# Kernel optimization log

Hardware: AMD Instinct MI355X
Metric: run time of the kernel (lower is better)

## Reference

```python
import jax, jax.numpy as jnp
import numpy as np

N_NODES = 100000


def gcn_conv(x, W, b, src, dst, num_nodes):
    """PyG GCNConv: out = D^{-1/2} (A + I) D^{-1/2} (x W) + b, messages src->dst."""
    h = x @ W  # [N, out]
    # degree with self-loops (edge weight 1)
    deg = jax.ops.segment_sum(jnp.ones(src.shape[0], dtype=x.dtype), dst,
                              num_segments=num_nodes) + 1.0
    dinv = jax.lax.rsqrt(deg)  # [N]
    norm = dinv[src] * dinv[dst]  # [E]
    msg = h[src] * norm[:, None]  # gather + scale, [E, out]
    agg = jax.ops.segment_sum(msg, dst, num_segments=num_nodes)
    # self-loop term: norm_ii = dinv[i]^2
    agg = agg + h * (dinv * dinv)[:, None]
    return agg + b


def setup_inputs() -> dict:
    key = jax.random.key(0)
    ks = jax.random.split(key, 9)
    N, F_in, H1, H2, C = N_NODES, 128, 64, 32, 10
    E = 3200000
    feature = jax.random.normal(ks[0], (N, F_in), dtype=jnp.float32)
    edge_index = jax.random.randint(ks[1], (2, E), 0, N, dtype=jnp.int64)
    def glorot(k, shape):
        lim = np.sqrt(6.0 / (shape[0] + shape[1]))
        return jax.random.uniform(k, shape, jnp.float32, -lim, lim)
    return {
        "feature": feature,
        "edge_index": edge_index,
        "W1": glorot(ks[2], (F_in, H1)),
        "b1": jnp.zeros((H1,), jnp.float32),
        "W2": glorot(ks[3], (H1, H2)),
        "b2": jnp.zeros((H2,), jnp.float32),
        "Wc": glorot(ks[4], (H2, C)),
        "bc": jnp.zeros((C,), jnp.float32),
    }


def reference(feature, edge_index, W1, b1, W2, b2, Wc, bc):
    src, dst = edge_index[0], edge_index[1]
    x = gcn_conv(feature, W1, b1, src, dst, N_NODES)
    x = jax.nn.relu(x)
    # dropout is identity in eval mode
    x = gcn_conv(x, W2, b2, src, dst, N_NODES)
    x = jax.nn.relu(x)
    logits = x @ Wc + bc
    return jax.nn.log_softmax(logits, axis=1)
```

## Files before the change

### kernel.cpp

```cpp
#include <hip/hip_runtime.h>

#define N_NODES 100000
#define F_IN 128
#define H1 64
#define H2 32
#define NCLS 10

#define BS_N 256
#define NBUCK ((N_NODES + BS_N - 1) / BS_N)
#define LCAP 32
#define MCAP 9216
#define OVCAP 6144
#define STCAP 9216
#define BIN_WG 256

__device__ __forceinline__ unsigned short f2bf(float f) {
    unsigned int u = __float_as_uint(f);
    return (unsigned short)((u + 0x7fffu + ((u >> 16) & 1u)) >> 16);
}
__device__ __forceinline__ float bf2f(unsigned short u) {
    return __uint_as_float((unsigned int)u << 16);
}
__device__ __forceinline__ void accp(float* a, unsigned int u) {
    a[0] += __uint_as_float(u << 16);
    a[1] += __uint_as_float(u & 0xffff0000u);
}
__device__ __forceinline__ void accp4(float* a, uint4 v) {
    accp(a + 0, v.x); accp(a + 2, v.y); accp(a + 4, v.z); accp(a + 6, v.w);
}

__global__ __launch_bounds__(512) void bin_kernel(const int* __restrict__ src,
                                                  const int* __restrict__ dst, int E,
                                                  unsigned int* __restrict__ gcur,
                                                  unsigned int* __restrict__ mainr,
                                                  unsigned int* __restrict__ ovcnt,
                                                  unsigned int* __restrict__ ovbuf) {
    __shared__ unsigned int buf[NBUCK][LCAP];
    __shared__ int cnt[NBUCK];
    int tid = threadIdx.x;
    for (int b = tid; b < NBUCK; b += 512) cnt[b] = 0;

    int chunk = (E + gridDim.x - 1) / gridDim.x;
    int e_lo = blockIdx.x * chunk;
    int e_hi = min(e_lo + chunk, E);

    int d0 = 0, s0 = 0, d1 = 0, s1 = 0;
    {
        int ea = e_lo + tid, eb = e_lo + 512 + tid;
        if (ea < e_hi) { d0 = dst[ea]; s0 = src[ea]; }
        if (eb < e_hi) { d1 = dst[eb]; s1 = src[eb]; }
    }
    __syncthreads();

    for (int base = e_lo; base < e_hi; base += 1024) {
        if (base + tid < e_hi) {
            int b = d0 >> 8;
            unsigned int en = ((unsigned int)s0 << 8) | (unsigned int)(d0 & 255);
            int p = atomicAdd(&cnt[b], 1);
            if (p < LCAP) buf[b][p] = en;
            else {
                unsigned int op = atomicAdd(&ovcnt[b * 16], 1u);
                if (op < OVCAP) ovbuf[(size_t)b * OVCAP + op] = en;
            }
        }
        if (base + 512 + tid < e_hi) {
            int b = d1 >> 8;
            unsigned int en = ((unsigned int)s1 << 8) | (unsigned int)(d1 & 255);
            int p = atomicAdd(&cnt[b], 1);
            if (p < LCAP) buf[b][p] = en;
            else {
                unsigned int op = atomicAdd(&ovcnt[b * 16], 1u);
                if (op < OVCAP) ovbuf[(size_t)b * OVCAP + op] = en;
            }
        }
        __syncthreads();
        {
            int nb = base + 1024;
            int ea = nb + tid, eb = nb + 512 + tid;
            if (ea < e_hi) { d0 = dst[ea]; s0 = src[ea]; }
            if (eb < e_hi) { d1 = dst[eb]; s1 = src[eb]; }
        }
        for (int b = tid; b < NBUCK; b += 512) {
            int c = cnt[b]; if (c > LCAP) c = LCAP;
            int nf = c & ~15;
            if (nf) {
                unsigned int gb = atomicAdd(&gcur[b * 16], (unsigned int)nf);
                if (gb + (unsigned)nf <= MCAP) {
                    for (int k = 0; k < nf; k += 4) {
                        uint4 v = make_uint4(buf[b][k], buf[b][k + 1],
                                             buf[b][k + 2], buf[b][k + 3]);
                        *(uint4*)&mainr[(size_t)b * MCAP + gb + k] = v;
                    }
                } else {
                    unsigned int op = atomicAdd(&ovcnt[b * 16], (unsigned int)nf);
                    for (int k = 0; k < nf; ++k)
                        if (op + k < OVCAP) ovbuf[(size_t)b * OVCAP + op + k] = buf[b][k];
                }
                int rem = c - nf;
                for (int k = 0; k < rem; ++k) buf[b][k] = buf[b][nf + k];
                cnt[b] = rem;
            } else {
                cnt[b] = c;
            }
        }
        __syncthreads();
    }
    for (int b = tid; b < NBUCK; b += 512) {
        int c = cnt[b]; if (c > LCAP) c = LCAP;
        if (c) {
            unsigned int ob = atomicAdd(&ovcnt[b * 16], (unsigned int)c);
            for (int k = 0; k < c; ++k)
                if (ob + k < OVCAP) ovbuf[(size_t)b * OVCAP + ob + k] = buf[b][k];
        }
    }
}

__global__ __launch_bounds__(256) void build_kernel(const unsigned int* __restrict__ gcur,
                                                    unsigned int* __restrict__ mainr,
                                                    const unsigned int* __restrict__ ovcnt,
                                                    const unsigned int* __restrict__ ovbuf,
                                                    float* __restrict__ dinv,
                                                    int* __restrict__ row_start,
                                                    int* __restrict__ row_end) {
    __shared__ unsigned int stage[STCAP];
    __shared__ int degl[BS_N];
    __shared__ int rs_l[BS_N];
    __shared__ int curl[BS_N];
    __shared__ int wtot[4];
    int b = blockIdx.x;
    int tid = threadIdx.x;

    int cm = (int)gcur[b * 16]; if (cm > MCAP) cm = MCAP;
    for (int i = tid; i < cm; i += 256) stage[i] = mainr[(size_t)b * MCAP + i];
    int co = (int)ovcnt[b * 16]; if (co > OVCAP) co = OVCAP;
    for (int i = tid; i < co; i += 256) {
        int p = cm + i;
        if (p < STCAP) stage[p] = ovbuf[(size_t)b * OVCAP + i];
    }
    int c = cm + co; if (c > STCAP) c = STCAP;
    degl[tid] = 0;
    __syncthreads();

    for (int i = tid; i < c; i += 256) atomicAdd(&degl[stage[i] & 255], 1);
    __syncthreads();

    int lane = tid & 63, w = tid >> 6;
    int d = degl[tid];
    int x = d;
    #pragma unroll
    for (int off = 1; off < 64; off <<= 1) {
        int y = __shfl_up(x, off);
        if (lane >= off) x += y;
    }
    if (lane == 63) wtot[w] = x;
    __syncthreads();
    int pbase = 0;
    #pragma unroll
    for (int k = 0; k < 4; ++k) if (k < w) pbase += wtot[k];
    rs_l[tid] = pbase + x - d;
    curl[tid] = 0;
    __syncthreads();

    size_t gbase = (size_t)b * MCAP;
    for (int i = tid; i < c; i += 256) {
        unsigned int en = stage[i];
        int dl = en & 255;
        int p = atomicAdd(&curl[dl], 1);
        mainr[gbase + rs_l[dl] + p] = en >> 8;
    }
    int node = b * BS_N + tid;
    if (node < N_NODES) {
        int deg = degl[tid];
        dinv[node] = rsqrtf((float)deg + 1.0f);
        row_start[node] = (int)gbase + rs_l[tid];
        row_end[node] = (int)gbase + rs_l[tid] + deg;
    }
}

__global__ __launch_bounds__(256) void gemm1_kernel(const float* __restrict__ X,
                                                    const float* __restrict__ W,
                                                    const float* __restrict__ dinv,
                                                    unsigned short* __restrict__ H) {
    __shared__ float Xs[64][68];
    __shared__ float Ws[F_IN * H1];
    int r0 = blockIdx.x * 64;
    const float4* W4 = (const float4*)W;
    float4* Ws4 = (float4*)Ws;
    for (int i = threadIdx.x; i < F_IN * H1 / 4; i += 256) Ws4[i] = W4[i];

    int tx = threadIdx.x & 15;
    int ty = threadIdx.x >> 4;
    float acc[4][4] = {};

    for (int kh = 0; kh < 2; ++kh) {
        __syncthreads();
        for (int it = 0; it < 4; ++it) {
            int idx = threadIdx.x + it * 256;
            int r = idx >> 4, k4 = idx & 15;
            int row = r0 + r;
            float4 v = (row < N_NODES)
                ? ((const float4*)X)[(size_t)row * 32 + kh * 16 + k4]
                : make_float4(0.f, 0.f, 0.f, 0.f);
            *(float4*)&Xs[r][k4 * 4] = v;
        }
        __syncthreads();
        #pragma unroll 8
        for (int k = 0; k < 64; ++k) {
            float4 wb = *(const float4*)&Ws[(kh * 64 + k) * H1 + tx * 4];
            float xa0 = Xs[ty * 4 + 0][k];
            float xa1 = Xs[ty * 4 + 1][k];
            float xa2 = Xs[ty * 4 + 2][k];
            float xa3 = Xs[ty * 4 + 3][k];
            acc[0][0] += xa0 * wb.x; acc[0][1] += xa0 * wb.y; acc[0][2] += xa0 * wb.z; acc[0][3] += xa0 * wb.w;
            acc[1][0] += xa1 * wb.x; acc[1][1] += xa1 * wb.y; acc[1][2] += xa1 * wb.z; acc[1][3] += xa1 * wb.w;
            acc[2][0] += xa2 * wb.x; acc[2][1] += xa2 * wb.y; acc[2][2] += xa2 * wb.z; acc[2][3] += xa2 * wb.w;
            acc[3][0] += xa3 * wb.x; acc[3][1] += xa3 * wb.y; acc[3][2] += xa3 * wb.z; acc[3][3] += xa3 * wb.w;
        }
    }
    #pragma unroll
    for (int i = 0; i < 4; ++i) {
        int row = r0 + ty * 4 + i;
        if (row < N_NODES) {
            float dv = dinv[row];
            unsigned int lo = (unsigned int)f2bf(acc[i][0] * dv) |
                              ((unsigned int)f2bf(acc[i][1] * dv) << 16);
            unsigned int hi = (unsigned int)f2bf(acc[i][2] * dv) |
                              ((unsigned int)f2bf(acc[i][3] * dv) << 16);
            *(uint2*)&H[(size_t)row * H1 + tx * 4] = make_uint2(lo, hi);
        }
    }
}

__global__ __launch_bounds__(256) void gemm2_kernel(const float* __restrict__ X,
                                                    const float* __restrict__ W,
                                                    const float* __restrict__ dinv,
                                                    unsigned short* __restrict__ H) {
    __shared__ float Xs[64][68];
    __shared__ float Ws[H1 * H2];
    int r0 = blockIdx.x * 64;
    const float4* W4 = (const float4*)W;
    float4* Ws4 = (float4*)Ws;
    for (int i = threadIdx.x; i < H1 * H2 / 4; i += 256) Ws4[i] = W4[i];
    for (int it = 0; it < 4; ++it) {
        int idx = threadIdx.x + it * 256;
        int r = idx >> 4, k4 = idx & 15;
        int row = r0 + r;
        float4 v = (row < N_NODES)
            ? ((const float4*)X)[(size_t)row * 16 + k4]
            : make_float4(0.f, 0.f, 0.f, 0.f);
        *(float4*)&Xs[r][k4 * 4] = v;
    }
    __syncthreads();
    int tx = threadIdx.x & 15;
    int ty = threadIdx.x >> 4;
    float acc[4][2] = {};
    #pragma unroll 8
    for (int k = 0; k < 64; ++k) {
        float2 wb = *(const float2*)&Ws[k * H2 + tx * 2];
        float xa0 = Xs[ty * 4 + 0][k];
        float xa1 = Xs[ty * 4 + 1][k];
        float xa2 = Xs[ty * 4 + 2][k];
        float xa3 = Xs[ty * 4 + 3][k];
        acc[0][0] += xa0 * wb.x; acc[0][1] += xa0 * wb.y;
        acc[1][0] += xa1 * wb.x; acc[1][1] += xa1 * wb.y;
        acc[2][0] += xa2 * wb.x; acc[2][1] += xa2 * wb.y;
        acc[3][0] += xa3 * wb.x; acc[3][1] += xa3 * wb.y;
    }
    #pragma unroll
    for (int i = 0; i < 4; ++i) {
        int row = r0 + ty * 4 + i;
        if (row < N_NODES) {
            float dv = dinv[row];
            unsigned int v = (unsigned int)f2bf(acc[i][0] * dv) |
                             ((unsigned int)f2bf(acc[i][1] * dv) << 16);
            *(unsigned int*)&H[(size_t)row * H2 + tx * 2] = v;
        }
    }
}

__global__ __launch_bounds__(256) void pull1_kernel(const unsigned short* __restrict__ h,
                                                    const unsigned int* __restrict__ csr,
                                                    const int* __restrict__ row_start,
                                                    const int* __restrict__ row_end,
                                                    const float* __restrict__ dinv,
                                                    const float* __restrict__ b,
                                                    float* __restrict__ xout) {
    int wave = (blockIdx.x * 256 + threadIdx.x) >> 6;
    int lane = threadIdx.x & 63;
    int g = lane >> 3;
    int sub = lane & 7;
    int i = wave;
    int e0 = row_start[i], e1 = row_end[i];
    float acc[8] = {};
    int e = e0;
    for (; e + 16 <= e1; e += 16) {
        int s0 = csr[e + g];
        int s1 = csr[e + 8 + g];
        uint4 v0 = *(const uint4*)&h[(size_t)s0 * H1 + sub * 8];
        uint4 v1 = *(const uint4*)&h[(size_t)s1 * H1 + sub * 8];
        accp4(acc, v0);
        accp4(acc, v1);
    }
    if (e + 8 <= e1) {
        int s = csr[e + g];
        uint4 v = *(const uint4*)&h[(size_t)s * H1 + sub * 8];
        accp4(acc, v);
        e += 8;
    }
    if (e < e1) {
        int idx = e + g;
        if (idx < e1) {
            int s = csr[idx];
            uint4 v = *(const uint4*)&h[(size_t)s * H1 + sub * 8];
            accp4(acc, v);
        }
    }
    #pragma unroll
    for (int m = 8; m < 64; m <<= 1) {
        #pragma unroll
        for (int j = 0; j < 8; ++j) acc[j] += __shfl_xor(acc[j], m);
    }
    if (g == 0) {
        float di = dinv[i];
        uint4 sv = *(const uint4*)&h[(size_t)i * H1 + sub * 8];
        accp4(acc, sv);
        float4 o0, o1;
        o0.x = fmaxf(di * acc[0] + b[sub * 8 + 0], 0.0f);
        o0.y = fmaxf(di * acc[1] + b[sub * 8 + 1], 0.0f);
        o0.z = fmaxf(di * acc[2] + b[sub * 8 + 2], 0.0f);
        o0.w = fmaxf(di * acc[3] + b[sub * 8 + 3], 0.0f);
        o1.x = fmaxf(di * acc[4] + b[sub * 8 + 4], 0.0f);
        o1.y = fmaxf(di * acc[5] + b[sub * 8 + 5], 0.0f);
        o1.z = fmaxf(di * acc[6] + b[sub * 8 + 6], 0.0f);
        o1.w = fmaxf(di * acc[7] + b[sub * 8 + 7], 0.0f);
        *(float4*)&xout[(size_t)i * H1 + sub * 8] = o0;
        *(float4*)&xout[(size_t)i * H1 + sub * 8 + 4] = o1;
    }
}

__global__ __launch_bounds__(256) void pull2_kernel(const unsigned short* __restrict__ h,
                                                    const unsigned int* __restrict__ csr,
                                                    const int* __restrict__ row_start,
                                                    const int* __restrict__ row_end,
                                                    const float* __restrict__ dinv,
                                                    const float* __restrict__ b,
                                                    float* __restrict__ xout) {
    int wave = (blockIdx.x * 256 + threadIdx.x) >> 6;
    int lane = threadIdx.x & 63;
    int g = lane >> 2;
    int sub = lane & 3;
    int i = wave;
    int e0 = row_start[i], e1 = row_end[i];
    float acc[8] = {};
    int e = e0;
    for (; e + 32 <= e1; e += 32) {
        int s0 = csr[e + g];
        int s1 = csr[e + 16 + g];
        uint4 v0 = *(const uint4*)&h[(size_t)s0 * H2 + sub * 8];
        uint4 v1 = *(const uint4*)&h[(size_t)s1 * H2 + sub * 8];
        accp4(acc, v0);
        accp4(acc, v1);
    }
    if (e + 16 <= e1) {
        int s = csr[e + g];
        uint4 v = *(const uint4*)&h[(size_t)s * H2 + sub * 8];
        accp4(acc, v);
        e += 16;
    }
    if (e < e1) {
        int idx = e + g;
        if (idx < e1) {
            int s = csr[idx];
            uint4 v = *(const uint4*)&h[(size_t)s * H2 + sub * 8];
            accp4(acc, v);
        }
    }
    #pragma unroll
    for (int m = 4; m < 64; m <<= 1) {
        #pragma unroll
        for (int j = 0; j < 8; ++j) acc[j] += __shfl_xor(acc[j], m);
    }
    if (g == 0) {
        float di = dinv[i];
        uint4 sv = *(const uint4*)&h[(size_t)i * H2 + sub * 8];
        accp4(acc, sv);
        float4 o0, o1;
        o0.x = fmaxf(di * acc[0] + b[sub * 8 + 0], 0.0f);
        o0.y = fmaxf(di * acc[1] + b[sub * 8 + 1], 0.0f);
        o0.z = fmaxf(di * acc[2] + b[sub * 8 + 2], 0.0f);
        o0.w = fmaxf(di * acc[3] + b[sub * 8 + 3], 0.0f);
        o1.x = fmaxf(di * acc[4] + b[sub * 8 + 4], 0.0f);
        o1.y = fmaxf(di * acc[5] + b[sub * 8 + 5], 0.0f);
        o1.z = fmaxf(di * acc[6] + b[sub * 8 + 6], 0.0f);
        o1.w = fmaxf(di * acc[7] + b[sub * 8 + 7], 0.0f);
        *(float4*)&xout[(size_t)i * H2 + sub * 8] = o0;
        *(float4*)&xout[(size_t)i * H2 + sub * 8 + 4] = o1;
    }
}

__global__ __launch_bounds__(256) void final_kernel(const float* __restrict__ X2,
                                                    const float* __restrict__ Wc,
                                                    const float* __restrict__ bc,
                                                    float* __restrict__ out) {
    __shared__ float Ws[H2 * NCLS];
    __shared__ float bs[NCLS];
    for (int idx = threadIdx.x; idx < H2 * NCLS; idx += 256) Ws[idx] = Wc[idx];
    if (threadIdx.x < NCLS) bs[threadIdx.x] = bc[threadIdx.x];
    __syncthreads();
    int i = blockIdx.x * blockDim.x + threadIdx.x;
    if (i >= N_NODES) return;
    float x[H2];
    #pragma unroll
    for (int k = 0; k < H2; ++k) x[k] = X2[(size_t)i * H2 + k];
    float lg[NCLS];
    #pragma unroll
    for (int c = 0; c < NCLS; ++c) {
        float acc = bs[c];
        #pragma unroll
        for (int k = 0; k < H2; ++k) acc += x[k] * Ws[k * NCLS + c];
        lg[c] = acc;
    }
    float m = lg[0];
    #pragma unroll
    for (int c = 1; c < NCLS; ++c) m = fmaxf(m, lg[c]);
    float s = 0.0f;
    #pragma unroll
    for (int c = 0; c < NCLS; ++c) s += expf(lg[c] - m);
    float lse = m + logf(s);
    #pragma unroll
    for (int c = 0; c < NCLS; ++c) out[(size_t)i * NCLS + c] = lg[c] - lse;
}

extern "C" void kernel_launch(void* const* d_in, const int* in_sizes, int n_in,
                              void* d_out, int out_size, void* d_ws, size_t ws_size,
                              hipStream_t stream) {
    const float* feature = (const float*)d_in[0];
    const int*   eidx    = (const int*)d_in[1];
    const float* W1      = (const float*)d_in[2];
    const float* b1      = (const float*)d_in[3];
    const float* W2      = (const float*)d_in[4];
    const float* b2      = (const float*)d_in[5];
    const float* Wc      = (const float*)d_in[6];
    const float* bc      = (const float*)d_in[7];
    float* out = (float*)d_out;

    const int E = in_sizes[1] / 2;
    const int* src = eidx;
    const int* dst = eidx + E;

    float*          ws        = (float*)d_ws;
    float*          dinv      = ws;
    int*            row_start = (int*)(dinv + N_NODES);
    int*            row_end   = row_start + N_NODES;
    unsigned int*   gcur      = (unsigned int*)(row_end + N_NODES);
    unsigned int*   ovcnt     = gcur + (size_t)NBUCK * 16;
    unsigned int*   ovbuf     = ovcnt + (size_t)NBUCK * 16;
    unsigned int*   mainr     = ovbuf + (size_t)NBUCK * OVCAP;
    unsigned short* h1b       = (unsigned short*)(mainr + (size_t)NBUCK * MCAP);
    float*          x1        = (float*)(h1b + (size_t)N_NODES * H1);
    unsigned short* h2b       = h1b;
    float*          x2        = x1;

    hipMemsetAsync(gcur, 0, (size_t)NBUCK * 32 * sizeof(unsigned int), stream);
    bin_kernel<<<BIN_WG, 512, 0, stream>>>(src, dst, E, gcur, mainr, ovcnt, ovbuf);
    build_kernel<<<NBUCK, 256, 0, stream>>>(gcur, mainr, ovcnt, ovbuf,
                                            dinv, row_start, row_end);

    gemm1_kernel<<<(N_NODES + 63) / 64, 256, 0, stream>>>(feature, W1, dinv, h1b);
    {
        unsigned int grid = (unsigned int)(((size_t)N_NODES * 64 + 255) / 256);
        pull1_kernel<<<grid, 256, 0, stream>>>(h1b, mainr, row_start, row_end, dinv, b1, x1);
    }

    gemm2_kernel<<<(N_NODES + 63) / 64, 256, 0, stream>>>(x1, W2, dinv, h2b);
    {
        unsigned int grid = (unsigned int)(((size_t)N_NODES * 64 + 255) / 256);
        pull2_kernel<<<grid, 256, 0, stream>>>(h2b, mainr, row_start, row_end, dinv, b2, x2);
    }

    final_kernel<<<(N_NODES + 255) / 256, 256, 0, stream>>>(x2, Wc, bc, out);
}
```

Before: 311.4 us.

## Fuse classifier and log-softmax into second aggregation; flush bin leftovers to main region

```diff
diff --git a/kernel.cpp b/kernel.cpp
--- a/kernel.cpp
+++ b/kernel.cpp
@@ -9,17 +9,15 @@
 #define BS_N 256
 #define NBUCK ((N_NODES + BS_N - 1) / BS_N)
 #define LCAP 32
-#define MCAP 9216
-#define OVCAP 6144
-#define STCAP 9216
+#define MCAP 12288
+#define OVCAP 2048
+#define STCAP 12288
 #define BIN_WG 256
+#define SENT 0xFFFFFFFFu
 
 __device__ __forceinline__ unsigned short f2bf(float f) {
     unsigned int u = __float_as_uint(f);
     return (unsigned short)((u + 0x7fffu + ((u >> 16) & 1u)) >> 16);
-}
-__device__ __forceinline__ float bf2f(unsigned short u) {
-    return __uint_as_float((unsigned int)u << 16);
 }
 __device__ __forceinline__ void accp(float* a, unsigned int u) {
     a[0] += __uint_as_float(u << 16);
@@ -108,9 +106,20 @@
     for (int b = tid; b < NBUCK; b += 512) {
         int c = cnt[b]; if (c > LCAP) c = LCAP;
         if (c) {
-            unsigned int ob = atomicAdd(&ovcnt[b * 16], (unsigned int)c);
-            for (int k = 0; k < c; ++k)
-                if (ob + k < OVCAP) ovbuf[(size_t)b * OVCAP + ob + k] = buf[b][k];
+            int cp = (c + 15) & ~15;
+            for (int k = c; k < cp; ++k) buf[b][k] = SENT;
+            unsigned int gb = atomicAdd(&gcur[b * 16], (unsigned int)cp);
+            if (gb + (unsigned)cp <= MCAP) {
+                for (int k = 0; k < cp; k += 4) {
+                    uint4 v = make_uint4(buf[b][k], buf[b][k + 1],
+                                         buf[b][k + 2], buf[b][k + 3]);
+                    *(uint4*)&mainr[(size_t)b * MCAP + gb + k] = v;
+                }
+            } else {
+                unsigned int op = atomicAdd(&ovcnt[b * 16], (unsigned int)c);
+                for (int k = 0; k < c; ++k)
+                    if (op + k < OVCAP) ovbuf[(size_t)b * OVCAP + op + k] = buf[b][k];
+            }
         }
     }
 }
@@ -141,7 +150,10 @@
     degl[tid] = 0;
     __syncthreads();
 
-    for (int i = tid; i < c; i += 256) atomicAdd(&degl[stage[i] & 255], 1);
+    for (int i = tid; i < c; i += 256) {
+        unsigned int en = stage[i];
+        if (en != SENT) atomicAdd(&degl[en & 255], 1);
+    }
     __syncthreads();
 
     int lane = tid & 63, w = tid >> 6;
@@ -164,9 +176,11 @@
     size_t gbase = (size_t)b * MCAP;
     for (int i = tid; i < c; i += 256) {
         unsigned int en = stage[i];
-        int dl = en & 255;
-        int p = atomicAdd(&curl[dl], 1);
-        mainr[gbase + rs_l[dl] + p] = en >> 8;
+        if (en != SENT) {
+            int dl = en & 255;
+            int p = atomicAdd(&curl[dl], 1);
+            mainr[gbase + rs_l[dl] + p] = en >> 8;
+        }
     }
     int node = b * BS_N + tid;
     if (node < N_NODES) {
@@ -343,8 +357,22 @@
                                                     const int* __restrict__ row_start,
                                                     const int* __restrict__ row_end,
                                                     const float* __restrict__ dinv,
-                                                    const float* __restrict__ b,
-                                                    float* __restrict__ xout) {
+                                                    const float* __restrict__ b2,
+                                                    const float* __restrict__ Wc,
+                                                    const float* __restrict__ bc,
+                                                    float* __restrict__ out) {
+    __shared__ float Wcs[336];
+    __shared__ float b2s[32];
+    __shared__ float bcs[16];
+    for (int t = threadIdx.x; t < 336; t += 256)
+        Wcs[t] = (t < H2 * NCLS) ? Wc[t] : 0.0f;
+    {
+        int t = threadIdx.x;
+        if (t < 32) b2s[t] = b2[t];
+        if (t < 16) bcs[t] = (t < NCLS) ? bc[t] : 0.0f;
+    }
+    __syncthreads();
+
     int wave = (blockIdx.x * 256 + threadIdx.x) >> 6;
     int lane = threadIdx.x & 63;
     int g = lane >> 2;
@@ -380,55 +408,29 @@
         #pragma unroll
         for (int j = 0; j < 8; ++j) acc[j] += __shfl_xor(acc[j], m);
     }
-    if (g == 0) {
-        float di = dinv[i];
-        uint4 sv = *(const uint4*)&h[(size_t)i * H2 + sub * 8];
-        accp4(acc, sv);
-        float4 o0, o1;
-        o0.x = fmaxf(di * acc[0] + b[sub * 8 + 0], 0.0f);
-        o0.y = fmaxf(di * acc[1] + b[sub * 8 + 1], 0.0f);
-        o0.z = fmaxf(di * acc[2] + b[sub * 8 + 2], 0.0f);
-        o0.w = fmaxf(di * acc[3] + b[sub * 8 + 3], 0.0f);
-        o1.x = fmaxf(di * acc[4] + b[sub * 8 + 4], 0.0f);
-        o1.y = fmaxf(di * acc[5] + b[sub * 8 + 5], 0.0f);
-        o1.z = fmaxf(di * acc[6] + b[sub * 8 + 6], 0.0f);
-        o1.w = fmaxf(di * acc[7] + b[sub * 8 + 7], 0.0f);
-        *(float4*)&xout[(size_t)i * H2 + sub * 8] = o0;
-        *(float4*)&xout[(size_t)i * H2 + sub * 8 + 4] = o1;
-    }
-}
-
-__global__ __launch_bounds__(256) void final_kernel(const float* __restrict__ X2,
-                                                    const float* __restrict__ Wc,
-                                                    const float* __restrict__ bc,
-                                                    float* __restrict__ out) {
-    __shared__ float Ws[H2 * NCLS];
-    __shared__ float bs[NCLS];
-    for (int idx = threadIdx.x; idx < H2 * NCLS; idx += 256) Ws[idx] = Wc[idx];
-    if (threadIdx.x < NCLS) bs[threadIdx.x] = bc[threadIdx.x];
-    __syncthreads();
-    int i = blockIdx.x * blockDim.x + threadIdx.x;
-    if (i >= N_NODES) return;
-    float x[H2];
-    #pragma unroll
-    for (int k = 0; k < H2; ++k) x[k] = X2[(size_t)i * H2 + k];
-    float lg[NCLS];
-    #pragma unroll
-    for (int c = 0; c < NCLS; ++c) {
-        float acc = bs[c];
-        #pragma unroll
-        for (int k = 0; k < H2; ++k) acc += x[k] * Ws[k * NCLS + c];
-        lg[c] = acc;
-    }
-    float m = lg[0];
-    #pragma unroll
-    for (int c = 1; c < NCLS; ++c) m = fmaxf(m, lg[c]);
-    float s = 0.0f;
-    #pragma unroll
-    for (int c = 0; c < NCLS; ++c) s += expf(lg[c] - m);
-    float lse = m + logf(s);
-    #pragma unroll
-    for (int c = 0; c < NCLS; ++c) out[(size_t)i * NCLS + c] = lg[c] - lse;
+    float di = dinv[i];
+    uint4 sv = *(const uint4*)&h[(size_t)i * H2 + sub * 8];
+    accp4(acc, sv);
+    float x2v[8];
+    #pragma unroll
+    for (int j = 0; j < 8; ++j)
+        x2v[j] = fmaxf(di * acc[j] + b2s[sub * 8 + j], 0.0f);
+
+    int c = lane & 15;
+    float lg = bcs[c];
+    #pragma unroll
+    for (int k = 0; k < H2; ++k) {
+        float xv = __shfl(x2v[k & 7], k >> 3);
+        lg += xv * Wcs[k * NCLS + c];
+    }
+    float mval = (c < NCLS) ? lg : -3.4e38f;
+    #pragma unroll
+    for (int m = 1; m < 16; m <<= 1) mval = fmaxf(mval, __shfl_xor(mval, m));
+    float ex = (c < NCLS) ? expf(lg - mval) : 0.0f;
+    #pragma unroll
+    for (int m = 1; m < 16; m <<= 1) ex += __shfl_xor(ex, m);
+    float o = lg - mval - logf(ex);
+    if (lane < NCLS) out[(size_t)i * NCLS + lane] = o;
 }
 
 extern "C" void kernel_launch(void* const* d_in, const int* in_sizes, int n_in,
@@ -459,7 +461,6 @@
     unsigned short* h1b       = (unsigned short*)(mainr + (size_t)NBUCK * MCAP);
     float*          x1        = (float*)(h1b + (size_t)N_NODES * H1);
     unsigned short* h2b       = h1b;
-    float*          x2        = x1;
 
     hipMemsetAsync(gcur, 0, (size_t)NBUCK * 32 * sizeof(unsigned int), stream);
     bin_kernel<<<BIN_WG, 512, 0, stream>>>(src, dst, E, gcur, mainr, ovcnt, ovbuf);
@@ -475,8 +476,7 @@
     gemm2_kernel<<<(N_NODES + 63) / 64, 256, 0, stream>>>(x1, W2, dinv, h2b);
     {
         unsigned int grid = (unsigned int)(((size_t)N_NODES * 64 + 255) / 256);
-        pull2_kernel<<<grid, 256, 0, stream>>>(h2b, mainr, row_start, row_end, dinv, b2, x2);
-    }
-
-    final_kernel<<<(N_NODES + 255) / 256, 256, 0, stream>>>(x2, Wc, bc, out);
-}
+        pull2_kernel<<<grid, 256, 0, stream>>>(h2b, mainr, row_start, row_end, dinv,
+                                               b2, Wc, bc, out);
+    }
+}
```

Result: slower. 361.2 us (+16.0%).
